# Kernel optimization log

Hardware: AMD Instinct MI355X
Metric: run time of the kernel (lower is better)

## Reference

```python
import jax, jax.numpy as jnp
import numpy as np

EPS = 1e-6
N_HEAD, N_KV_HEAD = 16, 4
VE_GATE_CH = 12

def rmsnorm(x):
    return x * jax.lax.rsqrt(jnp.mean(x * x, axis=-1, keepdims=True) + EPS)

def apply_rotary_emb(x, cos, sin):
    half = x.shape[-1] // 2
    x1, x2 = x[..., :half], x[..., half:]
    return jnp.concatenate([x1 * cos + x2 * sin, -x1 * sin + x2 * cos], axis=-1)

def setup_inputs():
    key = jax.random.key(0)
    ks = jax.random.split(key, 8)
    B, S, D = 2, 2048, 1024
    H, KVH = N_HEAD, N_KV_HEAD
    hd = D // H
    x = jax.random.normal(ks[0], (B, S, D), jnp.float32)
    ve = jax.random.normal(ks[1], (B, S, KVH * hd), jnp.float32)
    # real rotary tables, broadcastable over [B,S,H,hd//2]
    inv_freq = 1.0 / (10000.0 ** (np.arange(hd // 2, dtype=np.float32) / (hd // 2)))
    ang = np.arange(S, dtype=np.float32)[:, None] * inv_freq[None, :]  # [S, hd//2]
    cos = jnp.asarray(np.cos(ang))[:, None, :]  # [S,1,hd//2]
    sin = jnp.asarray(np.sin(ang))[:, None, :]
    std = 0.02
    Wq = jax.random.normal(ks[2], (D, H * hd), jnp.float32) * std
    Wk = jax.random.normal(ks[3], (D, KVH * hd), jnp.float32) * std
    Wv = jax.random.normal(ks[4], (D, KVH * hd), jnp.float32) * std
    Wo = jax.random.normal(ks[5], (D, D), jnp.float32) * std
    Wg = jax.random.normal(ks[6], (VE_GATE_CH, KVH), jnp.float32) * std
    return {"x": x, "ve": ve, "cos": cos, "sin": sin, "Wq": Wq, "Wk": Wk,
            "Wv": Wv, "Wo": Wo, "Wg": Wg, "window_size": 512}

def reference(x, ve, cos, sin, Wq, Wk, Wv, Wo, Wg, window_size):
    B, S, D = x.shape
    H, KVH = N_HEAD, N_KV_HEAD
    hd = D // H
    q = (x @ Wq).reshape(B, S, H, hd)
    k = (x @ Wk).reshape(B, S, KVH, hd)
    v = (x @ Wv).reshape(B, S, KVH, hd)
    # value-embedding gating
    gate = 3.0 * jax.nn.sigmoid(x[..., :VE_GATE_CH] @ Wg)  # [B,S,KVH]
    v = v + gate[..., None] * ve.reshape(B, S, KVH, hd)
    # RoPE + QK rmsnorm * 1.2
    q = rmsnorm(apply_rotary_emb(q, cos, sin)) * 1.2
    k = rmsnorm(apply_rotary_emb(k, cos, sin)) * 1.2
    # GQA head repeat (repeat_interleave over head dim)
    rep = H // KVH
    k = jnp.repeat(k, rep, axis=2)  # [B,S,H,hd]
    v = jnp.repeat(v, rep, axis=2)
    scale = 1.0 / np.sqrt(hd).astype(np.float32)
    scores = jnp.einsum('bqhd,bkhd->bhqk', q, k) * scale  # [B,H,S,S]
    pos = jnp.arange(S)
    allow = (pos[None, :] <= pos[:, None]) & (pos[None, :] >= pos[:, None] - window_size + 1)
    scores = jnp.where(allow[None, None], scores, -jnp.inf)
    attn = jax.nn.softmax(scores, axis=-1)
    y = jnp.einsum('bhqk,bkhd->bqhd', attn, v).reshape(B, S, D)
    return y @ Wo
```

## Files before the change

kernel.cpp:

```cpp
#include <hip/hip_runtime.h>
#include <hip/hip_bf16.h>
#include <cstddef>
#include <cstdint>


typedef short v8s __attribute__((ext_vector_type(8)));
typedef float v4f __attribute__((ext_vector_type(4)));

__device__ __forceinline__ ushort b1(float a) {
  uint u = __float_as_uint(a);
  return (ushort)((u + 0x7FFFu + ((u >> 16) & 1u)) >> 16);
}
__device__ __forceinline__ uint bpack(float lo, float hi) {
  uint ul = __float_as_uint(lo), uh = __float_as_uint(hi);
  ul = (ul + 0x7FFFu + ((ul >> 16) & 1u)) >> 16;
  uh = (uh + 0x7FFFu + ((uh >> 16) & 1u)) & 0xFFFF0000u;
  return ul | uh;
}

__device__ __forceinline__ void async16(const ushort* g, ushort* l) {
  __builtin_amdgcn_global_load_lds(
      (__attribute__((address_space(1))) void*)(uintptr_t)(const void*)g,
      (__attribute__((address_space(3))) void*)(uintptr_t)(void*)l, 16, 0, 0);
}

__global__ __launch_bounds__(256) void prep_all(
    const float* __restrict__ x, ushort* __restrict__ xb,
    const float* __restrict__ Wg, float* __restrict__ gates,
    const float* __restrict__ cosp, const float* __restrict__ sinp,
    float2* __restrict__ cs,
    const float* __restrict__ Wq, const float* __restrict__ Wk,
    const float* __restrict__ Wv, const float* __restrict__ Wo,
    ushort* __restrict__ Wqt, ushort* __restrict__ Wkt,
    ushort* __restrict__ Wvt, ushort* __restrict__ Wot)
{
  const int bx = blockIdx.x, t = threadIdx.x;
  if (bx < 4096) {
    const float* row = x + (size_t)bx * 1024;
    float4 v = *(const float4*)(row + t * 4);
    ushort4 o;
    o.x = b1(v.x); o.y = b1(v.y); o.z = b1(v.z); o.w = b1(v.w);
    *(ushort4*)(xb + (size_t)bx * 1024 + t * 4) = o;
    if (t < 4) {
      float g = 0.f;
#pragma unroll
      for (int i = 0; i < 12; ++i) g += row[i] * Wg[i * 4 + t];
      gates[bx * 4 + t] = 3.0f / (1.0f + __expf(-g));
    }
    return;
  }
  if (bx < 4352) {
    const int i = (bx - 4096) * 256 + t;
    cs[i] = make_float2(cosp[i], sinp[i]);
    return;
  }
  __shared__ ushort tile[32][33];
  int u = bx - 4352;
  const float* W; ushort* Wt; int N, xx, yy;
  if (u < 1024)      { W = Wq; Wt = Wqt; N = 1024; xx = u & 31; yy = u >> 5; }
  else if (u < 2048) { u -= 1024; W = Wo; Wt = Wot; N = 1024; xx = u & 31; yy = u >> 5; }
  else if (u < 2304) { u -= 2048; W = Wk; Wt = Wkt; N = 256;  xx = u & 7;  yy = u >> 3; }
  else               { u -= 2304; W = Wv; Wt = Wvt; N = 256;  xx = u & 7;  yy = u >> 3; }
  const int n0 = xx * 32, k0 = yy * 32;
  const int tx = t & 31, ty = t >> 5;
#pragma unroll
  for (int i = 0; i < 4; ++i) {
    const int k = ty + i * 8;
    tile[k][tx] = b1(W[(size_t)(k0 + k) * N + n0 + tx]);
  }
  __syncthreads();
#pragma unroll
  for (int i = 0; i < 4; ++i) {
    const int n = ty + i * 8;
    Wt[(size_t)(n0 + n) * 1024 + k0 + tx] = tile[tx][n];
  }
}

__device__ __forceinline__ void gemm_mainloop(
    const ushort* __restrict__ A, const ushort* __restrict__ Bt,
    int K, int m0, int n0, ushort (*As)[64], ushort (*Bs)[64],
    v4f acc[2][4])
{
  const int t = threadIdx.x;
  const int lane = t & 63, wave = t >> 6;
  const int wr = wave >> 1, wc = wave & 1;
  const int quad = lane >> 4, l16 = lane & 15;
  const int l8 = lane >> 3;
  const int c8s = ((lane & 7) ^ l8) * 8;
  const int sc = (l16 & 7) * 8;

  const ushort* ap[2];
  ushort* al[2];
#pragma unroll
  for (int i = 0; i < 2; ++i) {
    const int row = wave * 8 + i * 32 + l8;
    ap[i] = A + (size_t)(m0 + row) * K + c8s;
    al[i] = &As[wave * 8 + i * 32][0];
  }
  const ushort* bp[4];
  ushort* bl[4];
#pragma unroll
  for (int i = 0; i < 4; ++i) {
    const int row = (wave * 4 + i) * 8 + l8;
    bp[i] = Bt + (size_t)(n0 + row) * K + c8s;
    bl[i] = &Bs[(wave * 4 + i) * 8][0];
  }

  auto stage = [&](int buf, int k0) {
#pragma unroll
    for (int i = 0; i < 2; ++i) async16(ap[i] + k0, al[i] + buf * (64 * 64));
#pragma unroll
    for (int i = 0; i < 4; ++i) async16(bp[i] + k0, bl[i] + buf * (128 * 64));
  };
  auto compute = [&](int buf) {
#pragma unroll
    for (int ks = 0; ks < 2; ++ks) {
      const int col = (ks * 32 + quad * 8) ^ sc;
      v8s af[2], bf[4];
#pragma unroll
      for (int i = 0; i < 2; ++i)
        af[i] = *(const v8s*)&As[buf * 64 + wr * 32 + i * 16 + l16][col];
#pragma unroll
      for (int i = 0; i < 4; ++i)
        bf[i] = *(const v8s*)&Bs[buf * 128 + wc * 64 + i * 16 + l16][col];
#pragma unroll
      for (int mt = 0; mt < 2; ++mt)
#pragma unroll
        for (int nt = 0; nt < 4; ++nt)
          acc[mt][nt] = __builtin_amdgcn_mfma_f32_16x16x32_bf16(
              af[mt], bf[nt], acc[mt][nt], 0, 0, 0);
    }
  };

  stage(0, 0);
  __syncthreads();
  int buf = 0;
  for (int k0 = 64; k0 < K; k0 += 64) {
    stage(buf ^ 1, k0);
    compute(buf);
    __syncthreads();
    buf ^= 1;
  }
  compute(buf);
}

__device__ __forceinline__ void gemm_mainloop32(
    const ushort* __restrict__ A, const ushort* __restrict__ Bt,
    int K, int m0, int n0, ushort (*As)[64], ushort (*Bs)[64],
    v4f acc[4])
{
  const int t = threadIdx.x;
  const int lane = t & 63, wave = t >> 6;
  const int wr = wave >> 1, wc = wave & 1;
  const int quad = lane >> 4, l16 = lane & 15;
  const int l8 = lane >> 3;
  const int c8s = ((lane & 7) ^ l8) * 8;
  const int sc = (l16 & 7) * 8;

  const ushort* ap = A + (size_t)(m0 + wave * 8 + l8) * K + c8s;
  ushort* al = &As[wave * 8][0];
  const ushort* bp[4];
  ushort* bl[4];
#pragma unroll
  for (int i = 0; i < 4; ++i) {
    const int row = (wave * 4 + i) * 8 + l8;
    bp[i] = Bt + (size_t)(n0 + row) * K + c8s;
    bl[i] = &Bs[(wave * 4 + i) * 8][0];
  }

  auto stage = [&](int buf, int k0) {
    async16(ap + k0, al + buf * (32 * 64));
#pragma unroll
    for (int i = 0; i < 4; ++i) async16(bp[i] + k0, bl[i] + buf * (128 * 64));
  };
  auto compute = [&](int buf) {
#pragma unroll
    for (int ks = 0; ks < 2; ++ks) {
      const int col = (ks * 32 + quad * 8) ^ sc;
      v8s af = *(const v8s*)&As[buf * 32 + wr * 16 + l16][col];
      v8s bf[4];
#pragma unroll
      for (int i = 0; i < 4; ++i)
        bf[i] = *(const v8s*)&Bs[buf * 128 + wc * 64 + i * 16 + l16][col];
#pragma unroll
      for (int nt = 0; nt < 4; ++nt)
        acc[nt] = __builtin_amdgcn_mfma_f32_16x16x32_bf16(af, bf[nt], acc[nt], 0, 0, 0);
    }
  };

  stage(0, 0);
  __syncthreads();
  int buf = 0;
  for (int k0 = 64; k0 < K; k0 += 64) {
    stage(buf ^ 1, k0);
    compute(buf);
    __syncthreads();
    buf ^= 1;
  }
  compute(buf);
}

__global__ __launch_bounds__(256) void gemm_qkv_fused(
    const ushort* __restrict__ A, const ushort* __restrict__ Bt,
    const float2* __restrict__ cs, const float* __restrict__ gates,
    const float* __restrict__ ve,
    ushort* __restrict__ qb, ushort* __restrict__ kb, ushort* __restrict__ vb)
{
  __shared__ ushort As[128][64];
  __shared__ ushort Bs[256][64];
  const int lin = blockIdx.y * 64 + blockIdx.x;
  const int swz = (lin & 7) * 96 + (lin >> 3);
  const int x8 = swz / 96, local = swz % 96;
  const int bxx = x8 * 8 + (local & 7), sec = local >> 3;
  const int m0 = bxx * 64, n0 = sec * 128;
  const int lane = threadIdx.x & 63, wave = threadIdx.x >> 6;
  const int wr = wave >> 1, wc = wave & 1;
  const int quad = lane >> 4, l16 = lane & 15;

  v4f acc[2][4];
#pragma unroll
  for (int i = 0; i < 2; ++i)
#pragma unroll
    for (int j = 0; j < 4; ++j) acc[i][j] = (v4f){0.f, 0.f, 0.f, 0.f};

  gemm_mainloop(A, Bt, 1024, m0, n0, As, Bs, acc);

  const int head_col = n0 + wc * 64;

  if (sec < 10) {
    const bool isQ = (sec < 8);
    const int h = (head_col - (isQ ? 0 : 1024)) >> 6;
    ushort* dst = isQ ? qb : kb;
    const int ld = isQ ? 1024 : 256;
#pragma unroll
    for (int mt = 0; mt < 2; ++mt)
#pragma unroll
      for (int r = 0; r < 4; ++r) {
        const int row = m0 + wr * 32 + mt * 16 + quad * 4 + r;
        const int s = row & 2047;
        const float2 cs0 = cs[s * 32 + l16];
        const float2 cs1 = cs[s * 32 + 16 + l16];
        const float x10 = acc[mt][0][r], x11 = acc[mt][1][r];
        const float x20 = acc[mt][2][r], x21 = acc[mt][3][r];
        float ss = x10 * x10 + x11 * x11 + x20 * x20 + x21 * x21;
        ss += __shfl_xor(ss, 1);
        ss += __shfl_xor(ss, 2);
        ss += __shfl_xor(ss, 4);
        ss += __shfl_xor(ss, 8);
        const float rs = rsqrtf(ss * (1.0f / 64.0f) + 1e-6f) * 1.2f;
        ushort* dp = dst + (size_t)row * ld + h * 64 + l16;
        dp[0]  = b1((x10 * cs0.x + x20 * cs0.y) * rs);
        dp[16] = b1((x11 * cs1.x + x21 * cs1.y) * rs);
        dp[32] = b1((-x10 * cs0.y + x20 * cs0.x) * rs);
        dp[48] = b1((-x11 * cs1.y + x21 * cs1.x) * rs);
      }
  } else {
    const int kvh = (head_col - 1280) >> 6;
#pragma unroll
    for (int mt = 0; mt < 2; ++mt)
#pragma unroll
      for (int r = 0; r < 4; ++r) {
        const int row = m0 + wr * 32 + mt * 16 + quad * 4 + r;
        const float gate = gates[row * 4 + kvh];
        const float* vep = ve + (size_t)row * 256 + kvh * 64 + l16;
        ushort* dp = vb + (size_t)row * 256 + kvh * 64 + l16;
#pragma unroll
        for (int nt = 0; nt < 4; ++nt)
          dp[nt * 16] = b1(acc[mt][nt][r] + gate * vep[nt * 16]);
      }
  }
}

__global__ __launch_bounds__(256) void gemm_wo(
    const ushort* __restrict__ A, const ushort* __restrict__ Bt,
    float* __restrict__ C)
{
  __shared__ ushort As[64][64];
  __shared__ ushort Bs[256][64];
  const int lin = blockIdx.y * 128 + blockIdx.x;
  const int swz = (lin & 7) * 128 + (lin >> 3);
  const int x8 = swz >> 7, local = swz & 127;
  const int bxx = x8 * 16 + (local & 15), byy = local >> 4;
  const int m0 = bxx * 32, n0 = byy * 128;
  const int lane = threadIdx.x & 63, wave = threadIdx.x >> 6;
  const int wr = wave >> 1, wc = wave & 1;
  const int quad = lane >> 4, l16 = lane & 15;

  v4f acc[4];
#pragma unroll
  for (int j = 0; j < 4; ++j) acc[j] = (v4f){0.f, 0.f, 0.f, 0.f};

  gemm_mainloop32(A, Bt, 1024, m0, n0, As, Bs, acc);

#pragma unroll
  for (int r = 0; r < 4; ++r) {
    float* cp = C + (size_t)(m0 + wr * 16 + quad * 4 + r) * 1024
                  + n0 + wc * 64 + l16;
#pragma unroll
    for (int nt = 0; nt < 4; ++nt) cp[nt * 16] = acc[nt][r];
  }
}

__global__ __launch_bounds__(256) void transpose_v(
    const ushort* __restrict__ vb, ushort* __restrict__ vtb)
{
  __shared__ ushort L[64][72];
  const int s0 = blockIdx.x * 64, kvh = blockIdx.y, b = blockIdx.z;
  const int t = threadIdx.x;
#pragma unroll
  for (int i = 0; i < 2; ++i) {
    const int cc = t + i * 256;
    const int srow = cc >> 3, c8 = (cc & 7) * 8;
    *(int4*)&L[srow][c8] =
        *(const int4*)(vb + ((size_t)(b * 2048 + s0 + srow)) * 256 + kvh * 64 + c8);
  }
  __syncthreads();
#pragma unroll
  for (int i = 0; i < 2; ++i) {
    const int cc = t + i * 256;
    const int drow = cc >> 3, s8 = (cc & 7) * 8;
    ushort w[8];
#pragma unroll
    for (int jj = 0; jj < 8; ++jj) w[jj] = L[s8 + jj][drow];
    *(int4*)(vtb + ((size_t)((b * 4 + kvh) * 64 + drow)) * 2048 + s0 + s8) =
        *(int4*)w;
  }
}

__global__ __launch_bounds__(256) void attn_mfma(
    const ushort* __restrict__ qb, const ushort* __restrict__ kb,
    const ushort* __restrict__ vtb, ushort* __restrict__ yb,
    const int* __restrict__ wptr)
{
  __shared__ ushort Ks[64][72];
  __shared__ ushort Vt[64][72];
  __shared__ ushort Ps[64][72];
  const int lin = (blockIdx.z * 16 + blockIdx.y) * 32 + blockIdx.x;
  const int swz = (lin & 7) * 128 + (lin >> 3);
  const int x8 = swz >> 7, local = swz & 127;
  const int qt = local & 31;
  const int hb = x8 * 4 + (local >> 5);
  const int h = hb & 15, b = hb >> 4;
  const int kvh = h >> 2, q0 = qt * 64;
  const int t = threadIdx.x, lane = t & 63, wave = t >> 6;
  const int quad = lane >> 4, l16 = lane & 15;
  const int Wwin = *wptr;

  v8s qf0, qf1;
  {
    const ushort* qp = qb + ((size_t)(b * 2048 + q0 + wave * 16 + l16)) * 1024
                          + h * 64 + quad * 8;
    qf0 = *(const v8s*)qp;
    qf1 = *(const v8s*)(qp + 32);
  }

  v8s vones;
#pragma unroll
  for (int i = 0; i < 8; ++i) vones[i] = (short)0x3F80;

  v4f o[5];
#pragma unroll
  for (int d = 0; d < 5; ++d) o[d] = (v4f){0.f, 0.f, 0.f, 0.f};

  const int lo = q0 - Wwin + 1;
  const int kt0 = (lo > 0) ? (lo >> 6) : 0;
  const int kt1 = (q0 + 63) >> 6;

  for (int kt = kt0; kt <= kt1; ++kt) {
#pragma unroll
    for (int i = 0; i < 2; ++i) {
      const int cc = t + i * 256;
      const int r8 = cc >> 3, c8 = (cc & 7) * 8;
      *(int4*)&Ks[r8][c8] =
          *(const int4*)(kb + ((size_t)(b * 2048 + kt * 64 + r8)) * 256 + kvh * 64 + c8);
      *(int4*)&Vt[r8][c8] =
          *(const int4*)(vtb + ((size_t)((b * 4 + kvh) * 64 + r8)) * 2048 + kt * 64 + c8);
    }
    __syncthreads();

    const bool needs_mask = (kt * 64 + 63 > q0) || (kt * 64 < q0 + 64 - Wwin);

    {
      const int qrow = q0 + wave * 16 + l16;
      ushort* prow = &Ps[wave * 16 + l16][0];
#pragma unroll
      for (int nt = 0; nt < 4; ++nt) {
        v8s kf0 = *(const v8s*)&Ks[nt * 16 + l16][quad * 8];
        v8s kf1 = *(const v8s*)&Ks[nt * 16 + l16][32 + quad * 8];
        v4f st = (v4f){0.f, 0.f, 0.f, 0.f};
        st = __builtin_amdgcn_mfma_f32_16x16x32_bf16(kf0, qf0, st, 0, 0, 0);
        st = __builtin_amdgcn_mfma_f32_16x16x32_bf16(kf1, qf1, st, 0, 0, 0);
        float p[4];
#pragma unroll
        for (int r = 0; r < 4; ++r) {
          p[r] = exp2f(fmaf(st[r], 0.18033688011f, -17.31234049107f));
          if (needs_mask) {
            const int k = kt * 64 + nt * 16 + quad * 4 + r;
            const bool ok = (k <= qrow) && (k > qrow - Wwin);
            p[r] = ok ? p[r] : 0.0f;
          }
        }
        uint2 w;
        w.x = bpack(p[0], p[1]);
        w.y = bpack(p[2], p[3]);
        *(uint2*)(prow + nt * 16 + quad * 4) = w;
      }
    }

    v8s pf0 = *(const v8s*)&Ps[wave * 16 + l16][quad * 8];
    v8s pf1 = *(const v8s*)&Ps[wave * 16 + l16][32 + quad * 8];
#pragma unroll
    for (int dt = 0; dt < 4; ++dt) {
      v8s vf0 = *(const v8s*)&Vt[dt * 16 + l16][quad * 8];
      v8s vf1 = *(const v8s*)&Vt[dt * 16 + l16][32 + quad * 8];
      o[dt] = __builtin_amdgcn_mfma_f32_16x16x32_bf16(pf0, vf0, o[dt], 0, 0, 0);
      o[dt] = __builtin_amdgcn_mfma_f32_16x16x32_bf16(pf1, vf1, o[dt], 0, 0, 0);
    }
    o[4] = __builtin_amdgcn_mfma_f32_16x16x32_bf16(pf0, vones, o[4], 0, 0, 0);
    o[4] = __builtin_amdgcn_mfma_f32_16x16x32_bf16(pf1, vones, o[4], 0, 0, 0);
    __syncthreads();
  }

#pragma unroll
  for (int r = 0; r < 4; ++r) {
    const float l = __shfl(o[4][r], lane & 48);
    const float inv = 1.0f / l;
    ushort* yp = yb + ((size_t)(b * 2048 + q0 + wave * 16 + quad * 4 + r)) * 1024
                    + h * 64 + l16;
#pragma unroll
    for (int dt = 0; dt < 4; ++dt) yp[dt * 16] = b1(o[dt][r] * inv);
  }
}

extern "C" void kernel_launch(void* const* d_in, const int* in_sizes, int n_in,
                              void* d_out, int out_size, void* d_ws, size_t ws_size,
                              hipStream_t stream)
{
  const float* x    = (const float*)d_in[0];
  const float* ve   = (const float*)d_in[1];
  const float* cosp = (const float*)d_in[2];
  const float* sinp = (const float*)d_in[3];
  const float* Wq   = (const float*)d_in[4];
  const float* Wk   = (const float*)d_in[5];
  const float* Wv   = (const float*)d_in[6];
  const float* Wo   = (const float*)d_in[7];
  const float* Wg   = (const float*)d_in[8];
  const int*   win  = (const int*)d_in[9];
  float* out = (float*)d_out;

  char* p = (char*)d_ws;
  ushort* xb    = (ushort*)p;  p += (size_t)4194304 * 2;
  ushort* qb    = (ushort*)p;  p += (size_t)4194304 * 2;
  ushort* yb    = (ushort*)p;  p += (size_t)4194304 * 2;
  ushort* kb    = (ushort*)p;  p += (size_t)1048576 * 2;
  ushort* vb    = (ushort*)p;  p += (size_t)1048576 * 2;
  ushort* vtb   = (ushort*)p;  p += (size_t)1048576 * 2;
  ushort* Wqkvt = (ushort*)p;  p += (size_t)1536 * 1024 * 2;
  ushort* Wot   = (ushort*)p;  p += (size_t)1048576 * 2;
  float2* cs    = (float2*)p;  p += (size_t)65536 * 8;
  float*  gates = (float*)p;

  prep_all<<<6912, 256, 0, stream>>>(
      x, xb, Wg, gates, cosp, sinp, cs, Wq, Wk, Wv, Wo,
      Wqkvt, Wqkvt + (size_t)1024 * 1024, Wqkvt + (size_t)1280 * 1024, Wot);

  gemm_qkv_fused<<<dim3(64, 12), 256, 0, stream>>>(xb, Wqkvt, cs, gates, ve,
                                                   qb, kb, vb);
  transpose_v<<<dim3(32, 4, 2), 256, 0, stream>>>(vb, vtb);

  attn_mfma<<<dim3(32, 16, 2), 256, 0, stream>>>(qb, kb, vtb, yb, win);

  gemm_wo<<<dim3(128, 8), 256, 0, stream>>>(yb, Wot, out);
}
```

Before: 160.4 us.

## Double-buffer K/V tiles in attention with register prefetch of next tile

The attention kernel now keeps two LDS buffers for K and V^T. It loads the next key tile into registers before computing the current tile, then writes it into the alternate buffer after the PV MFMAs, so global-load latency overlaps with compute. Each iteration now has one barrier instead of two. The cost is more LDS use and more registers, which may lower occupancy.

```diff
diff --git a/kernel.cpp b/kernel.cpp
--- a/kernel.cpp
+++ b/kernel.cpp
@@ -332,8 +332,8 @@
     const ushort* __restrict__ vtb, ushort* __restrict__ yb,
     const int* __restrict__ wptr)
 {
-  __shared__ ushort Ks[64][72];
-  __shared__ ushort Vt[64][72];
+  __shared__ ushort Ks[2][64][72];
+  __shared__ ushort Vt[2][64][72];
   __shared__ ushort Ps[64][72];
   const int lin = (blockIdx.z * 16 + blockIdx.y) * 32 + blockIdx.x;
   const int swz = (lin & 7) * 128 + (lin >> 3);
@@ -366,17 +366,33 @@
   const int kt0 = (lo > 0) ? (lo >> 6) : 0;
   const int kt1 = (q0 + 63) >> 6;
 
+  const int r8 = t >> 3, c8t = (t & 7) * 8;
+  const ushort* kbase = kb + ((size_t)(b * 2048 + r8)) * 256 + kvh * 64 + c8t;
+  const ushort* vbase = vtb + ((size_t)((b * 4 + kvh) * 64 + r8)) * 2048 + c8t;
+
+  int4 kr[2], vr[2];
+#pragma unroll
+  for (int i = 0; i < 2; ++i) {
+    kr[i] = *(const int4*)(kbase + (size_t)(kt0 * 64 + i * 32) * 256);
+    vr[i] = *(const int4*)(vbase + (size_t)(i * 32) * 2048 + kt0 * 64);
+  }
+#pragma unroll
+  for (int i = 0; i < 2; ++i) {
+    *(int4*)&Ks[0][r8 + i * 32][c8t] = kr[i];
+    *(int4*)&Vt[0][r8 + i * 32][c8t] = vr[i];
+  }
+  __syncthreads();
+
+  int pb = 0;
   for (int kt = kt0; kt <= kt1; ++kt) {
-#pragma unroll
-    for (int i = 0; i < 2; ++i) {
-      const int cc = t + i * 256;
-      const int r8 = cc >> 3, c8 = (cc & 7) * 8;
-      *(int4*)&Ks[r8][c8] =
-          *(const int4*)(kb + ((size_t)(b * 2048 + kt * 64 + r8)) * 256 + kvh * 64 + c8);
-      *(int4*)&Vt[r8][c8] =
-          *(const int4*)(vtb + ((size_t)((b * 4 + kvh) * 64 + r8)) * 2048 + kt * 64 + c8);
-    }
-    __syncthreads();
+    const bool more = (kt < kt1);
+    if (more) {
+#pragma unroll
+      for (int i = 0; i < 2; ++i) {
+        kr[i] = *(const int4*)(kbase + (size_t)((kt + 1) * 64 + i * 32) * 256);
+        vr[i] = *(const int4*)(vbase + (size_t)(i * 32) * 2048 + (kt + 1) * 64);
+      }
+    }
 
     const bool needs_mask = (kt * 64 + 63 > q0) || (kt * 64 < q0 + 64 - Wwin);
 
@@ -385,8 +401,8 @@
       ushort* prow = &Ps[wave * 16 + l16][0];
 #pragma unroll
       for (int nt = 0; nt < 4; ++nt) {
-        v8s kf0 = *(const v8s*)&Ks[nt * 16 + l16][quad * 8];
-        v8s kf1 = *(const v8s*)&Ks[nt * 16 + l16][32 + quad * 8];
+        v8s kf0 = *(const v8s*)&Ks[pb][nt * 16 + l16][quad * 8];
+        v8s kf1 = *(const v8s*)&Ks[pb][nt * 16 + l16][32 + quad * 8];
         v4f st = (v4f){0.f, 0.f, 0.f, 0.f};
         st = __builtin_amdgcn_mfma_f32_16x16x32_bf16(kf0, qf0, st, 0, 0, 0);
         st = __builtin_amdgcn_mfma_f32_16x16x32_bf16(kf1, qf1, st, 0, 0, 0);
@@ -411,14 +427,23 @@
     v8s pf1 = *(const v8s*)&Ps[wave * 16 + l16][32 + quad * 8];
 #pragma unroll
     for (int dt = 0; dt < 4; ++dt) {
-      v8s vf0 = *(const v8s*)&Vt[dt * 16 + l16][quad * 8];
-      v8s vf1 = *(const v8s*)&Vt[dt * 16 + l16][32 + quad * 8];
+      v8s vf0 = *(const v8s*)&Vt[pb][dt * 16 + l16][quad * 8];
+      v8s vf1 = *(const v8s*)&Vt[pb][dt * 16 + l16][32 + quad * 8];
       o[dt] = __builtin_amdgcn_mfma_f32_16x16x32_bf16(pf0, vf0, o[dt], 0, 0, 0);
       o[dt] = __builtin_amdgcn_mfma_f32_16x16x32_bf16(pf1, vf1, o[dt], 0, 0, 0);
     }
     o[4] = __builtin_amdgcn_mfma_f32_16x16x32_bf16(pf0, vones, o[4], 0, 0, 0);
     o[4] = __builtin_amdgcn_mfma_f32_16x16x32_bf16(pf1, vones, o[4], 0, 0, 0);
-    __syncthreads();
+
+    if (more) {
+#pragma unroll
+      for (int i = 0; i < 2; ++i) {
+        *(int4*)&Ks[pb ^ 1][r8 + i * 32][c8t] = kr[i];
+        *(int4*)&Vt[pb ^ 1][r8 + i * 32][c8t] = vr[i];
+      }
+      __syncthreads();
+      pb ^= 1;
+    }
   }
 
 #pragma unroll
```

Result: slower. 185.8 us (+15.8%).
